# Optimization experiments

Hardware: AMD Instinct MI355X
Metric: run time of the kernel (lower is better)

The kernel has to match this reference:

```python
import jax, jax.numpy as jnp
import numpy as np

B, V, D = 4096, 20, 768


def _conv1d_k3(x, w, b):
    # x: [B, V, D]; single-channel conv1d, kernel=3, padding=1 (torch cross-correlation)
    xp = jnp.pad(x, ((0, 0), (0, 0), (1, 1)))
    return w[0] * xp[..., :-2] + w[1] * xp[..., 1:-1] + w[2] * xp[..., 2:] + b[0]


def setup_inputs() -> dict:
    key = jax.random.key(0)
    ks = jax.random.split(key, 10)
    s = 0.02  # small init scale for weights
    return {
        "text_features": jax.random.normal(ks[0], (B, D), jnp.float32),
        "viewport_features": jax.random.normal(ks[1], (B, V, D), jnp.float32),
        "W1": jax.random.normal(ks[2], (D, D), jnp.float32) * s,
        "b1": jax.random.normal(ks[3], (D,), jnp.float32) * s,
        "W2": jax.random.normal(ks[4], (D, D), jnp.float32) * s,
        "b2": jax.random.normal(ks[5], (D,), jnp.float32) * s,
        "cw1": jax.random.normal(ks[6], (3,), jnp.float32) * 0.5,
        "cb1": jax.random.normal(ks[7], (1,), jnp.float32) * 0.1,
        "cw2": jax.random.normal(ks[8], (3,), jnp.float32) * 0.5,
        "cb2": jax.random.normal(ks[9], (1,), jnp.float32) * 0.1,
    }


def reference(text_features, viewport_features, W1, b1, W2, b2, cw1, cb1, cw2, cb2):
    # Batched over all 20 viewports at once (original loops over i).
    fli_norm = jax.nn.softmax(viewport_features, axis=-1)          # [B,V,D]
    # torch Linear: x @ W.T + b
    m1 = jnp.einsum('bvd,ed->bve', fli_norm, W1) + b1              # mlp1(fli_norm)
    m2 = jnp.einsum('bvd,ed->bve', fli_norm, W2) + b2              # mlp2(fli_norm)
    fused = jax.nn.relu(text_features[:, None, :] * m1 + m2)       # [B,V,D]
    fused = _conv1d_k3(fused, cw1, cb1)
    fused = jax.nn.relu(fused)
    fused = _conv1d_k3(fused, cw2, cb2)
    return fused.reshape(B, V * D)                                 # torch.cat along dim=1
```

## Files before the change

### kernel.cpp

```cpp
#include <hip/hip_runtime.h>

typedef unsigned short u16;
typedef unsigned char u8;
typedef __attribute__((ext_vector_type(8))) short short8;
typedef __attribute__((ext_vector_type(4))) float f32x4;
typedef __attribute__((ext_vector_type(2))) long long2v;

#define Bn 4096
#define Vn 20
#define Dn 768
#define Mn (Bn * Vn)
#define Nn (2 * Dn)

#define BM 256
#define BNt 256
#define NTILES (Nn / BNt)
#define GRID ((Mn / BM) * NTILES)
#define PANEL (256 * Dn)

#define SCL 32.0f
#define ISCL2 (1.0f / 1024.0f)

typedef __attribute__((address_space(1))) void GV;
typedef __attribute__((address_space(3))) void LV;

__device__ __forceinline__ u16 f2bf(float f) {
  union { float f; unsigned u; } v; v.f = f;
  unsigned r = v.u + 0x7FFFu + ((v.u >> 16) & 1u);
  return (u16)(r >> 16);
}
__device__ __forceinline__ float bf2f(u16 x) {
  union { unsigned u; float f; } v; v.u = ((unsigned)x) << 16; return v.f;
}


__global__ __launch_bounds__(512) void softmax_k(const float* __restrict__ vf,
                                                 u8* __restrict__ X8) {
  __shared__ __align__(16) u8 lds[24576];
  const int t = threadIdx.x;
  const int r = t >> 4;
  const int g = t & 15;
  const size_t q = (size_t)blockIdx.x * 32 + r;
  const float* src = vf + q * Dn + g * 4;
  float4 v[12];
  #pragma unroll
  for (int u = 0; u < 12; ++u) v[u] = *(const float4*)(src + u * 64);
  float mx = -1e30f;
  #pragma unroll
  for (int u = 0; u < 12; ++u)
    mx = fmaxf(mx, fmaxf(fmaxf(v[u].x, v[u].y), fmaxf(v[u].z, v[u].w)));
  #pragma unroll
  for (int off = 1; off < 16; off <<= 1) mx = fmaxf(mx, __shfl_xor(mx, off));
  float s = 0.f;
  #pragma unroll
  for (int u = 0; u < 12; ++u) {
    v[u].x = __expf(v[u].x - mx); v[u].y = __expf(v[u].y - mx);
    v[u].z = __expf(v[u].z - mx); v[u].w = __expf(v[u].w - mx);
    s += (v[u].x + v[u].y) + (v[u].z + v[u].w);
  }
  #pragma unroll
  for (int off = 1; off < 16; off <<= 1) s += __shfl_xor(s, off);
  const float inv = SCL / s;
  const int base = ((g >> 1) & 3) * 512 + r * 16 + (g >> 3) * 8 + (g & 1) * 4;
  #pragma unroll
  for (int u = 0; u < 12; ++u) {
    unsigned pk = 0;
    pk = __builtin_amdgcn_cvt_pk_fp8_f32(v[u].x * inv, v[u].y * inv, pk, false);
    pk = __builtin_amdgcn_cvt_pk_fp8_f32(v[u].z * inv, v[u].w * inv, pk, true);
    *(unsigned*)(lds + u * 2048 + base) = pk;
  }
  __syncthreads();
  u8* dst = X8 + (size_t)(blockIdx.x >> 3) * PANEL + (blockIdx.x & 7) * 512;
  #pragma unroll
  for (int rd = 0; rd < 3; ++rd) {
    const int o = (rd * 512 + t) * 16;
    const int chunk = o >> 9;
    *(uint4*)(dst + (chunk >> 2) * 16384 + (chunk & 3) * 4096 + (o & 511)) =
        *(const uint4*)(lds + o);
  }
}

__global__ __launch_bounds__(256) void build_wt_k(const float* __restrict__ W1,
                                                  const float* __restrict__ W2,
                                                  u8* __restrict__ Wt8) {
  int idx = blockIdx.x * 256 + threadIdx.x;
  if (idx >= Dn * (Dn / 4)) return;
  int j = idx / (Dn / 4), d4 = (idx - j * (Dn / 4)) * 4;
  int b = j >> 5, c = j & 31;
  float4 a = *(const float4*)(W1 + (size_t)j * Dn + d4);
  float4 e = *(const float4*)(W2 + (size_t)j * Dn + d4);
  unsigned p1 = 0, p2 = 0;
  p1 = __builtin_amdgcn_cvt_pk_fp8_f32(a.x * SCL, a.y * SCL, p1, false);
  p1 = __builtin_amdgcn_cvt_pk_fp8_f32(a.z * SCL, a.w * SCL, p1, true);
  p2 = __builtin_amdgcn_cvt_pk_fp8_f32(e.x * SCL, e.y * SCL, p2, false);
  p2 = __builtin_amdgcn_cvt_pk_fp8_f32(e.z * SCL, e.w * SCL, p2, true);
  const size_t off = (size_t)(d4 >> 6) * 16384 + ((d4 >> 3) & 3) * 4096
                   + ((d4 >> 5) & 1) * 8 + (d4 & 7);
  const int j1 = b * 64 + c, j2 = b * 64 + 32 + c;
  *(unsigned*)(Wt8 + (size_t)(j1 >> 8) * PANEL + off + (j1 & 255) * 16) = p1;
  *(unsigned*)(Wt8 + (size_t)(j2 >> 8) * PANEL + off + (j2 & 255) * 16) = p2;
}

__global__ __launch_bounds__(512, 2) void gemm_fuse_k(
    const u8* __restrict__ X8, const u8* __restrict__ Wt8,
    const float* __restrict__ b1, const float* __restrict__ b2,
    const float* __restrict__ text, float* __restrict__ out,
    u16* __restrict__ seam,
    const float* __restrict__ cw1, const float* __restrict__ cb1,
    const float* __restrict__ cw2, const float* __restrict__ cb2) {
  __shared__ __align__(16) u16 smem[65536];
  u8* smem8 = (u8*)smem;

  const int h = blockIdx.x;
  const int lin = (h & 7) * (GRID / 8) + (h >> 3);
  const int by = lin / NTILES, bx = lin - by * NTILES;
  const int brow = by * BM;

  const int t = threadIdx.x, w = t >> 6, l = t & 63;
  const int lo = l & 15, hi = l >> 4;
  const int wrr = w >> 2, wcc = w & 3;

  int offA[8], offB[4];
  #pragma unroll
  for (int m = 0; m < 8; ++m)
    offA[m] = hi * 4096 + (wrr * 128 + m * 16 + lo) * 16;
  #pragma unroll
  for (int n = 0; n < 4; ++n)
    offB[n] = 16384 + hi * 4096 + (wcc * 64 + n * 16 + lo) * 16;

  const u8* gAp = X8 + (size_t)by * PANEL + t * 16;
  const u8* gBp = Wt8 + (size_t)bx * PANEL + t * 16;

#define STG_A(SB, T) do {                                                      \
    __builtin_amdgcn_global_load_lds((GV*)(gAp + (size_t)(T) * 16384),         \
        (LV*)(smem8 + (SB) + w * 1024), 16, 0, 0);                             \
    __builtin_amdgcn_global_load_lds((GV*)(gAp + (size_t)(T) * 16384 + 8192),  \
        (LV*)(smem8 + (SB) + 8192 + w * 1024), 16, 0, 0); } while (0)
#define STG_B(SB, T) do {                                                      \
    __builtin_amdgcn_global_load_lds((GV*)(gBp + (size_t)(T) * 16384),         \
        (LV*)(smem8 + (SB) + 16384 + w * 1024), 16, 0, 0);                     \
    __builtin_amdgcn_global_load_lds((GV*)(gBp + (size_t)(T) * 16384 + 8192),  \
        (LV*)(smem8 + (SB) + 24576 + w * 1024), 16, 0, 0); } while (0)

  STG_A(0, 0);     STG_B(0, 0);
  STG_A(32768, 1); STG_B(32768, 1);
  asm volatile("s_waitcnt vmcnt(4)" ::: "memory");
  __builtin_amdgcn_s_barrier();

  f32x4 acc[8][4] = {};
  long2v af[8], bb[4];

  #pragma unroll
  for (int T = 0; T < 12; ++T) {
    const int cs = (T % 3) * 32768;
    const int ss = ((T + 2) % 3) * 32768;

    #pragma unroll
    for (int m = 0; m < 8; ++m)
      af[m] = *(const long2v*)(smem8 + cs + offA[m]);
    #pragma unroll
    for (int n = 0; n < 4; ++n)
      bb[n] = *(const long2v*)(smem8 + cs + offB[n]);
    if (T <= 9) { STG_A(ss, T + 2); STG_B(ss, T + 2); }
    __builtin_amdgcn_s_barrier();
    asm volatile("s_waitcnt lgkmcnt(0)" ::: "memory");
    __builtin_amdgcn_sched_barrier(0);
    __builtin_amdgcn_s_setprio(1);
    #pragma unroll
    for (int m = 0; m < 8; ++m) {
      #pragma unroll
      for (int n = 0; n < 4; ++n) {
        acc[m][n] = __builtin_amdgcn_mfma_f32_16x16x32_fp8_fp8(af[m][0], bb[n][0], acc[m][n], 0, 0, 0);
        acc[m][n] = __builtin_amdgcn_mfma_f32_16x16x32_fp8_fp8(af[m][1], bb[n][1], acc[m][n], 0, 0, 0);
      }
    }
    __builtin_amdgcn_s_setprio(0);
    if (T <= 9)       asm volatile("s_waitcnt vmcnt(4)" ::: "memory");
    else if (T == 10) asm volatile("s_waitcnt vmcnt(0)" ::: "memory");
    __builtin_amdgcn_s_barrier();
  }
#undef STG_A
#undef STG_B

  const float w10 = cw1[0], w11 = cw1[1], w12 = cw1[2], c1b = cb1[0];
  const float w20 = cw2[0], w21 = cw2[1], w22 = cw2[2], c2b = cb2[0];

  u16* fsm = smem;
  u16* tsm = smem + 32768;

  #pragma unroll
  for (int n = 0; n < 2; ++n) {
    const int cl = wcc * 32 + n * 16 + lo;
    const int e  = bx * 128 + cl;
    const float B1 = b1[e], B2 = b2[e];
    #pragma unroll
    for (int m = 0; m < 8; ++m) {
      const int rl = wrr * 128 + m * 16 + hi * 4;
      uint2 pk;
      u16* pku = (u16*)&pk;
      #pragma unroll
      for (int r = 0; r < 4; ++r) {
        const int gr = brow + rl + r;
        const float v1 = acc[m][n][r] * ISCL2 + B1;
        const float v2 = acc[m][n + 2][r] * ISCL2 + B2;
        const float tf = text[(size_t)(gr / Vn) * Dn + e];
        pku[r] = f2bf(fmaxf(tf * v1 + v2, 0.0f));
      }
      *(uint2*)(fsm + cl * 256 + (rl ^ ((cl & 31) << 3))) = pk;
      const int sidx = (cl < 4) ? cl : ((cl >= 124) ? cl - 120 : -1);
      if (sidx >= 0)
        *(uint2*)(seam + ((size_t)(by * 6 + bx) * 8 + sidx) * 256 + rl) = pk;
    }
  }
  __syncthreads();

  const int cl = t & 127, rb = t >> 7;
  const int cL = cl ? cl - 1 : 0, cR = (cl < 127) ? cl + 1 : 127;
  short8 tC[8];
  #pragma unroll
  for (int j = 0; j < 8; ++j) {
    const int R = rb * 64 + j * 8;
    short8 sL = *(const short8*)(fsm + cL * 256 + (R ^ ((cL & 31) << 3)));
    short8 sC = *(const short8*)(fsm + cl * 256 + (R ^ ((cl & 31) << 3)));
    short8 sR = *(const short8*)(fsm + cR * 256 + (R ^ ((cR & 31) << 3)));
    short8 o;
    #pragma unroll
    for (int k = 0; k < 8; ++k) {
      float a = bf2f((u16)sL[k]), b = bf2f((u16)sC[k]), c = bf2f((u16)sR[k]);
      float v = fmaxf(fmaf(w10, a, fmaf(w11, b, fmaf(w12, c, c1b))), 0.0f);
      o[k] = (short)f2bf(v);
    }
    *(short8*)(tsm + cl * 256 + (R ^ ((cl & 31) << 3))) = o;
    tC[j] = o;
  }
  __syncthreads();

  const bool wr_ok = (cl >= 2 && cl <= 125);
  #pragma unroll
  for (int j = 0; j < 8; ++j) {
    const int R = rb * 64 + j * 8;
    short8 tL = *(const short8*)(tsm + cL * 256 + (R ^ ((cL & 31) << 3)));
    short8 tR = *(const short8*)(tsm + cR * 256 + (R ^ ((cR & 31) << 3)));
    #pragma unroll
    for (int k = 0; k < 8; ++k) {
      float v = fmaf(w20, bf2f((u16)tL[k]),
                fmaf(w21, bf2f((u16)tC[j][k]),
                fmaf(w22, bf2f((u16)tR[k]), c2b)));
      if (wr_ok)
        out[(size_t)(brow + R + k) * Dn + bx * 128 + cl] = v;
    }
  }
}

__global__ __launch_bounds__(256) void seam_k(const u16* __restrict__ seam,
                                              float* __restrict__ out,
                                              const float* __restrict__ cw1,
                                              const float* __restrict__ cb1,
                                              const float* __restrict__ cw2,
                                              const float* __restrict__ cb2) {
  const int bid = blockIdx.x;
  const int by = bid / 6, bx = bid - by * 6;
  const int r = threadIdx.x;
  const float w10 = cw1[0], w11 = cw1[1], w12 = cw1[2], c1b = cb1[0];
  const float w20 = cw2[0], w21 = cw2[1], w22 = cw2[2], c2b = cb2[0];
  #define SM(B, I) bf2f(seam[((size_t)(B) * 8 + (I)) * 256 + r])
  float fm2 = 0.f, fm1 = 0.f, fR0 = 0.f, fR1 = 0.f;
  if (bx > 0) { fm2 = SM(bid - 1, 6); fm1 = SM(bid - 1, 7); }
  if (bx < 5) { fR0 = SM(bid + 1, 0); fR1 = SM(bid + 1, 1); }
  const float f0 = SM(bid, 0), f1 = SM(bid, 1), f2 = SM(bid, 2), f3 = SM(bid, 3);
  const float f124 = SM(bid, 4), f125 = SM(bid, 5), f126 = SM(bid, 6), f127 = SM(bid, 7);
  #undef SM
  #define C1(a, b, c) fmaxf(fmaf(w10, (a), fmaf(w11, (b), fmaf(w12, (c), c1b))), 0.0f)
  const float tm1  = (bx > 0) ? C1(fm2, fm1, f0) : 0.0f;
  const float t0   = C1(fm1, f0, f1);
  const float t1   = C1(f0, f1, f2);
  const float t2   = C1(f1, f2, f3);
  const float t125 = C1(f124, f125, f126);
  const float t126 = C1(f125, f126, f127);
  const float t127 = C1(f126, f127, fR0);
  const float t128 = (bx < 5) ? C1(f127, fR0, fR1) : 0.0f;
  #undef C1
  const size_t go = (size_t)(by * 256 + r) * Dn + bx * 128;
  out[go + 0]   = fmaf(w20, tm1,  fmaf(w21, t0,   fmaf(w22, t1,   c2b)));
  out[go + 1]   = fmaf(w20, t0,   fmaf(w21, t1,   fmaf(w22, t2,   c2b)));
  out[go + 126] = fmaf(w20, t125, fmaf(w21, t126, fmaf(w22, t127, c2b)));
  out[go + 127] = fmaf(w20, t126, fmaf(w21, t127, fmaf(w22, t128, c2b)));
}

extern "C" void kernel_launch(void* const* d_in, const int* in_sizes, int n_in,
                              void* d_out, int out_size, void* d_ws, size_t ws_size,
                              hipStream_t stream) {
  const float* text = (const float*)d_in[0];
  const float* vf   = (const float*)d_in[1];
  const float* W1   = (const float*)d_in[2];
  const float* b1   = (const float*)d_in[3];
  const float* W2   = (const float*)d_in[4];
  const float* b2   = (const float*)d_in[5];
  const float* cw1  = (const float*)d_in[6];
  const float* cb1  = (const float*)d_in[7];
  const float* cw2  = (const float*)d_in[8];
  const float* cb2  = (const float*)d_in[9];
  float* out = (float*)d_out;

  u8*  X8   = (u8*)d_ws;
  u8*  Wt8  = X8 + (size_t)Mn * Dn;
  u16* seam = (u16*)(Wt8 + (size_t)Nn * Dn);

  softmax_k<<<Mn / 32, 512, 0, stream>>>(vf, X8);
  build_wt_k<<<(Dn * (Dn / 4) + 255) / 256, 256, 0, stream>>>(W1, W2, Wt8);
  gemm_fuse_k<<<GRID, 512, 0, stream>>>(X8, Wt8, b1, b2, text, out, seam,
                                        cw1, cb1, cw2, cb2);
  seam_k<<<GRID, 256, 0, stream>>>(seam, out, cw1, cb1, cw2, cb2);
}
```

Before: 324.6 us.

## Switch projection GEMM from fp8 to int8 MFMA with per-row and weight scales

Replaces the fp8 16x16x32 MFMA pair with a single int8 16x16x64 MFMA per tile step. Inputs are quantized differently: unnormalized softmax exponentials are scaled by 127 and stored as int8, with per-row 1/sum saved. Weights are quantized symmetrically using a global abs-max, which two new kernels compute (a zero-init and an atomic max reduction). The epilogue rescales the int32 accumulators with the per-row and weight scales, and the fragment layouts in the softmax and weight-packing kernels are changed to match the 64-wide K chunks. The extra launches and per-row scale loads add overhead. Quantizing small softmax values to 127 levels may lose accuracy.

```diff
diff --git a/kernel.cpp b/kernel.cpp
--- a/kernel.cpp
+++ b/kernel.cpp
@@ -4,13 +4,14 @@
 typedef unsigned char u8;
 typedef __attribute__((ext_vector_type(8))) short short8;
 typedef __attribute__((ext_vector_type(4))) float f32x4;
-typedef __attribute__((ext_vector_type(2))) long long2v;
+typedef __attribute__((ext_vector_type(4))) int int4v;
 
 #define Bn 4096
 #define Vn 20
 #define Dn 768
 #define Mn (Bn * Vn)
 #define Nn (2 * Dn)
+#define NW (Dn * Dn)
 
 #define BM 256
 #define BNt 256
@@ -18,9 +19,6 @@
 #define GRID ((Mn / BM) * NTILES)
 #define PANEL (256 * Dn)
 
-#define SCL 32.0f
-#define ISCL2 (1.0f / 1024.0f)
-
 typedef __attribute__((address_space(1))) void GV;
 typedef __attribute__((address_space(3))) void LV;
 
@@ -34,14 +32,30 @@
 }
 
 
+__global__ void zero_k(unsigned* wm) { *wm = 0u; }
+
+__global__ __launch_bounds__(256) void wmax_k(const float* __restrict__ W1,
+                                              const float* __restrict__ W2,
+                                              unsigned* __restrict__ wm) {
+  float m = 0.f;
+  for (int i = blockIdx.x * 256 + threadIdx.x; i < 2 * NW; i += gridDim.x * 256) {
+    float a = fabsf(i < NW ? W1[i] : W2[i - NW]);
+    m = fmaxf(m, a);
+  }
+  #pragma unroll
+  for (int off = 32; off; off >>= 1) m = fmaxf(m, __shfl_xor(m, off));
+  if ((threadIdx.x & 63) == 0) atomicMax(wm, __float_as_uint(m));
+}
+
 __global__ __launch_bounds__(512) void softmax_k(const float* __restrict__ vf,
-                                                 u8* __restrict__ X8) {
+                                                 u8* __restrict__ X8,
+                                                 float* __restrict__ invs) {
   __shared__ __align__(16) u8 lds[24576];
   const int t = threadIdx.x;
   const int r = t >> 4;
   const int g = t & 15;
-  const size_t q = (size_t)blockIdx.x * 32 + r;
-  const float* src = vf + q * Dn + g * 4;
+  const size_t row = (size_t)blockIdx.x * 32 + r;
+  const float* src = vf + row * Dn + g * 4;
   float4 v[12];
   #pragma unroll
   for (int u = 0; u < 12; ++u) v[u] = *(const float4*)(src + u * 64);
@@ -60,14 +74,15 @@
   }
   #pragma unroll
   for (int off = 1; off < 16; off <<= 1) s += __shfl_xor(s, off);
-  const float inv = SCL / s;
-  const int base = ((g >> 1) & 3) * 512 + r * 16 + (g >> 3) * 8 + (g & 1) * 4;
+  if (g == 0) invs[row] = 1.0f / s;
+  const int base = (g >> 2) * 512 + r * 16 + (g & 3) * 4;
   #pragma unroll
   for (int u = 0; u < 12; ++u) {
-    unsigned pk = 0;
-    pk = __builtin_amdgcn_cvt_pk_fp8_f32(v[u].x * inv, v[u].y * inv, pk, false);
-    pk = __builtin_amdgcn_cvt_pk_fp8_f32(v[u].z * inv, v[u].w * inv, pk, true);
-    *(unsigned*)(lds + u * 2048 + base) = pk;
+    unsigned i0 = (unsigned)__float2int_rn(v[u].x * 127.f);
+    unsigned i1 = (unsigned)__float2int_rn(v[u].y * 127.f);
+    unsigned i2 = (unsigned)__float2int_rn(v[u].z * 127.f);
+    unsigned i3 = (unsigned)__float2int_rn(v[u].w * 127.f);
+    *(unsigned*)(lds + u * 2048 + base) = i0 | (i1 << 8) | (i2 << 16) | (i3 << 24);
   }
   __syncthreads();
   u8* dst = X8 + (size_t)(blockIdx.x >> 3) * PANEL + (blockIdx.x & 7) * 512;
@@ -82,20 +97,20 @@
 
 __global__ __launch_bounds__(256) void build_wt_k(const float* __restrict__ W1,
                                                   const float* __restrict__ W2,
-                                                  u8* __restrict__ Wt8) {
+                                                  u8* __restrict__ Wt8,
+                                                  const unsigned* __restrict__ wm) {
   int idx = blockIdx.x * 256 + threadIdx.x;
   if (idx >= Dn * (Dn / 4)) return;
+  const float aw = 127.0f / __uint_as_float(*wm);
   int j = idx / (Dn / 4), d4 = (idx - j * (Dn / 4)) * 4;
   int b = j >> 5, c = j & 31;
   float4 a = *(const float4*)(W1 + (size_t)j * Dn + d4);
   float4 e = *(const float4*)(W2 + (size_t)j * Dn + d4);
-  unsigned p1 = 0, p2 = 0;
-  p1 = __builtin_amdgcn_cvt_pk_fp8_f32(a.x * SCL, a.y * SCL, p1, false);
-  p1 = __builtin_amdgcn_cvt_pk_fp8_f32(a.z * SCL, a.w * SCL, p1, true);
-  p2 = __builtin_amdgcn_cvt_pk_fp8_f32(e.x * SCL, e.y * SCL, p2, false);
-  p2 = __builtin_amdgcn_cvt_pk_fp8_f32(e.z * SCL, e.w * SCL, p2, true);
-  const size_t off = (size_t)(d4 >> 6) * 16384 + ((d4 >> 3) & 3) * 4096
-                   + ((d4 >> 5) & 1) * 8 + (d4 & 7);
+  #define Q8(x) ((unsigned)(min(127, max(-127, __float2int_rn((x) * aw))) & 255))
+  unsigned p1 = Q8(a.x) | (Q8(a.y) << 8) | (Q8(a.z) << 16) | (Q8(a.w) << 24);
+  unsigned p2 = Q8(e.x) | (Q8(e.y) << 8) | (Q8(e.z) << 16) | (Q8(e.w) << 24);
+  #undef Q8
+  const size_t off = (size_t)(d4 >> 6) * 16384 + ((d4 >> 4) & 3) * 4096 + (d4 & 15);
   const int j1 = b * 64 + c, j2 = b * 64 + 32 + c;
   *(unsigned*)(Wt8 + (size_t)(j1 >> 8) * PANEL + off + (j1 & 255) * 16) = p1;
   *(unsigned*)(Wt8 + (size_t)(j2 >> 8) * PANEL + off + (j2 & 255) * 16) = p2;
@@ -105,7 +120,8 @@
     const u8* __restrict__ X8, const u8* __restrict__ Wt8,
     const float* __restrict__ b1, const float* __restrict__ b2,
     const float* __restrict__ text, float* __restrict__ out,
-    u16* __restrict__ seam,
+    u16* __restrict__ seam, const float* __restrict__ invs,
+    const unsigned* __restrict__ wmp,
     const float* __restrict__ cw1, const float* __restrict__ cb1,
     const float* __restrict__ cw2, const float* __restrict__ cb2) {
   __shared__ __align__(16) u16 smem[65536];
@@ -147,8 +163,8 @@
   asm volatile("s_waitcnt vmcnt(4)" ::: "memory");
   __builtin_amdgcn_s_barrier();
 
-  f32x4 acc[8][4] = {};
-  long2v af[8], bb[4];
+  int4v acc[8][4] = {};
+  int4v af[8], bb[4];
 
   #pragma unroll
   for (int T = 0; T < 12; ++T) {
@@ -157,23 +173,20 @@
 
     #pragma unroll
     for (int m = 0; m < 8; ++m)
-      af[m] = *(const long2v*)(smem8 + cs + offA[m]);
+      af[m] = *(const int4v*)(smem8 + cs + offA[m]);
     #pragma unroll
     for (int n = 0; n < 4; ++n)
-      bb[n] = *(const long2v*)(smem8 + cs + offB[n]);
+      bb[n] = *(const int4v*)(smem8 + cs + offB[n]);
     if (T <= 9) { STG_A(ss, T + 2); STG_B(ss, T + 2); }
     __builtin_amdgcn_s_barrier();
     asm volatile("s_waitcnt lgkmcnt(0)" ::: "memory");
     __builtin_amdgcn_sched_barrier(0);
     __builtin_amdgcn_s_setprio(1);
     #pragma unroll
-    for (int m = 0; m < 8; ++m) {
+    for (int m = 0; m < 8; ++m)
       #pragma unroll
-      for (int n = 0; n < 4; ++n) {
-        acc[m][n] = __builtin_amdgcn_mfma_f32_16x16x32_fp8_fp8(af[m][0], bb[n][0], acc[m][n], 0, 0, 0);
-        acc[m][n] = __builtin_amdgcn_mfma_f32_16x16x32_fp8_fp8(af[m][1], bb[n][1], acc[m][n], 0, 0, 0);
-      }
-    }
+      for (int n = 0; n < 4; ++n)
+        acc[m][n] = __builtin_amdgcn_mfma_i32_16x16x64_i8(af[m], bb[n], acc[m][n], 0, 0, 0);
     __builtin_amdgcn_s_setprio(0);
     if (T <= 9)       asm volatile("s_waitcnt vmcnt(4)" ::: "memory");
     else if (T == 10) asm volatile("s_waitcnt vmcnt(0)" ::: "memory");
@@ -184,6 +197,7 @@
 
   const float w10 = cw1[0], w11 = cw1[1], w12 = cw1[2], c1b = cb1[0];
   const float w20 = cw2[0], w21 = cw2[1], w22 = cw2[2], c2b = cb2[0];
+  const float wsc = __uint_as_float(*wmp) * (1.0f / 16129.0f);
 
   u16* fsm = smem;
   u16* tsm = smem + 32768;
@@ -201,8 +215,9 @@
       #pragma unroll
       for (int r = 0; r < 4; ++r) {
         const int gr = brow + rl + r;
-        const float v1 = acc[m][n][r] * ISCL2 + B1;
-        const float v2 = acc[m][n + 2][r] * ISCL2 + B2;
+        const float scr = invs[gr] * wsc;
+        const float v1 = (float)acc[m][n][r] * scr + B1;
+        const float v2 = (float)acc[m][n + 2][r] * scr + B2;
         const float tf = text[(size_t)(gr / Vn) * Dn + e];
         pku[r] = f2bf(fmaxf(tf * v1 + v2, 0.0f));
       }
@@ -305,10 +320,14 @@
   u8*  X8   = (u8*)d_ws;
   u8*  Wt8  = X8 + (size_t)Mn * Dn;
   u16* seam = (u16*)(Wt8 + (size_t)Nn * Dn);
-
-  softmax_k<<<Mn / 32, 512, 0, stream>>>(vf, X8);
-  build_wt_k<<<(Dn * (Dn / 4) + 255) / 256, 256, 0, stream>>>(W1, W2, Wt8);
+  float* invs = (float*)(seam + (size_t)GRID * 8 * 256);
+  unsigned* wm = (unsigned*)(invs + Mn);
+
+  zero_k<<<1, 1, 0, stream>>>(wm);
+  wmax_k<<<512, 256, 0, stream>>>(W1, W2, wm);
+  softmax_k<<<Mn / 32, 512, 0, stream>>>(vf, X8, invs);
+  build_wt_k<<<(Dn * (Dn / 4) + 255) / 256, 256, 0, stream>>>(W1, W2, Wt8, wm);
   gemm_fuse_k<<<GRID, 512, 0, stream>>>(X8, Wt8, b1, b2, text, out, seam,
-                                        cw1, cb1, cw2, cb2);
+                                        invs, wm, cw1, cb1, cw2, cb2);
   seam_k<<<GRID, 256, 0, stream>>>(seam, out, cw1, cb1, cw2, cb2);
 }
```

Result: no change. 325.0 us (+0.1%).
